# Kernel optimization log

Measured on AMD Instinct MI355X. Metric: run time of the kernel, lower is better.

The kernel has to match this reference:

```python
import jax, jax.numpy as jnp
import numpy as np

IN_DIMS = 1024
OUT_DIMS = 1024
N_TOKENS = 32768


def setup_inputs() -> dict:
    key = jax.random.key(0)
    k_x, k_wl0, k_wl1, k_scale, k_shift, k_noise = jax.random.split(key, 6)
    x = jax.random.normal(k_x, (N_TOKENS, IN_DIMS), dtype=jnp.float32)
    # weight_logits[..., 0]: magnitude logits, weight_logits[..., 1]: sign logits
    gain = np.sqrt(2.0)  # relu gain
    a = gain * np.sqrt(6.0 / (IN_DIMS + OUT_DIMS))
    mag_logits = jax.random.uniform(k_wl0, (OUT_DIMS, IN_DIMS), dtype=jnp.float32,
                                    minval=-a, maxval=a)  # logit(0.5)=0, so centered at 0
    sgn_logits = jax.random.uniform(k_wl1, (OUT_DIMS, IN_DIMS), dtype=jnp.float32,
                                    minval=-a, maxval=a)
    weight_logits = jnp.stack([mag_logits, sgn_logits], axis=-1)  # [O, I, 2]
    scale = jnp.full((OUT_DIMS,), np.float32(a), dtype=jnp.float32)
    shift = jnp.full((OUT_DIMS,), 0.01, dtype=jnp.float32)
    noise = jax.random.normal(k_noise, (N_TOKENS, OUT_DIMS), dtype=jnp.float32)
    return {"x": x, "weight_logits": weight_logits, "scale": scale,
            "shift": shift, "noise": noise}


def reference(x, weight_logits, scale, shift, noise):
    # train_forward of TernaryLinear
    weight_p = jax.nn.sigmoid(weight_logits)          # [O, I, 2]
    p_mag = weight_p[..., 0]                          # P(|w| = 1)
    p_sgn = weight_p[..., 1]                          # P(w > 0 | |w| = 1)
    s = 2.0 * p_sgn - 1.0
    weight_mean = p_mag * s                           # [O, I]
    weight_var = p_mag - (p_mag * p_mag) * (s * s)    # [O, I], >= 0
    out_mean = jnp.einsum('ni,oi->no', x, weight_mean)         # [N, O]
    out_var = jnp.einsum('ni,oi->no', x * x, weight_var)       # [N, O]
    out = out_mean + jnp.sqrt(out_var) * noise
    out = out * scale[None, :] + shift[None, :]
    return out
```

## Files before the change

### kernel.cpp

```cpp
#include <hip/hip_runtime.h>
#include <hip/hip_bf16.h>
#include <cmath>

#define N_TOK 32768
#define KDIM  1024
#define ODIM  1024

#define BM 256
#define BN 128
#define BK 64
#define NKT (KDIM / BK)
#define THREADS 512
#define BUFSZ 65536

typedef float          f32x4  __attribute__((ext_vector_type(4)));
typedef __bf16         bf16x8 __attribute__((ext_vector_type(8)));
typedef unsigned short us8    __attribute__((ext_vector_type(8)));
typedef unsigned short us2   __attribute__((ext_vector_type(2)));

static __device__ __forceinline__ unsigned short f2bf(float f) {
  unsigned u = __builtin_bit_cast(unsigned, f);
  u += 0x7FFFu + ((u >> 16) & 1u);
  return (unsigned short)(u >> 16);
}

static __device__ __forceinline__ unsigned short bfc(float f) {
  return __builtin_bit_cast(unsigned short, (__bf16)f);
}

static __device__ __forceinline__ f32x4 mfma16(us8 a, us8 b, f32x4 c) {
  return __builtin_amdgcn_mfma_f32_16x16x32_bf16(
      __builtin_bit_cast(bf16x8, a), __builtin_bit_cast(bf16x8, b), c, 0, 0, 0);
}

static __device__ __forceinline__ void gl_lds16(const void* g, void* l) {
  __builtin_amdgcn_global_load_lds(
      (const __attribute__((address_space(1))) void*)g,
      (__attribute__((address_space(3))) void*)l, 16, 0, 0);
}

static __device__ __forceinline__ us8 sqr8(us8 a) {
  us8 r;
#pragma unroll
  for (int i = 0; i < 8; ++i) {
    float f = __builtin_bit_cast(float, (unsigned)a[i] << 16);
    r[i] = bfc(f * f);
  }
  return r;
}

__global__ void wprep_kernel(const float* __restrict__ wl,
                             unsigned short* __restrict__ wm,
                             unsigned short* __restrict__ wv) {
  int i = blockIdx.x * blockDim.x + threadIdx.x;
  f32x4 v = *reinterpret_cast<const f32x4*>(wl + (size_t)i * 4);
  float pm0 = 1.f / (1.f + expf(-v.x));
  float ps0 = 1.f / (1.f + expf(-v.y));
  float pm1 = 1.f / (1.f + expf(-v.z));
  float ps1 = 1.f / (1.f + expf(-v.w));
  float m0 = pm0 * (2.f * ps0 - 1.f);
  float m1 = pm1 * (2.f * ps1 - 1.f);
  float q0 = pm0 - m0 * m0;
  float q1 = pm1 - m1 * m1;
  us2 am = {f2bf(m0), f2bf(m1)};
  us2 av = {f2bf(q0), f2bf(q1)};
  *reinterpret_cast<us2*>(wm + (size_t)i * 2) = am;
  *reinterpret_cast<us2*>(wv + (size_t)i * 2) = av;
}

__global__ __launch_bounds__(THREADS, 2) void ternary_gemm(
    const float* __restrict__ x,
    const unsigned short* __restrict__ wm,
    const unsigned short* __restrict__ wv,
    const float* __restrict__ scale,
    const float* __restrict__ shift,
    const float* __restrict__ noise,
    float* __restrict__ out) {
  __shared__ alignas(16) char smem[2 * BUFSZ];

  const int tid  = threadIdx.x;
  const int lane = tid & 63;
  const int w    = tid >> 6;
  const bool isVar = (w >= 4);
  const int p    = w & 3;
  const int wr   = p >> 1;
  const int wc   = p & 1;
  const int l15  = lane & 15;
  const int l4   = lane >> 4;

  const int bid = blockIdx.x;
  const int swz = (bid & 7) * 128 + (bid >> 3);
  const int bm  = swz >> 3;
  const int bn  = swz & 7;
  const int rowBase = bm * BM;
  const int colBase = bn * BN;

  f32x4 acc[8][4];
#pragma unroll
  for (int i = 0; i < 8; ++i)
#pragma unroll
    for (int j = 0; j < 4; ++j) acc[i][j] = (f32x4)0.f;

  const float* xb = x + (size_t)rowBase * KDIM;

  auto stageB = [&](int kt, char* buf) {
    const int k0 = kt * BK;
    char* BsM = buf + 32768;
    char* BsV = buf + 49152;
#pragma unroll
    for (int c = 0; c < 2; ++c) {
      int flat = c * THREADS + tid;
      int row  = flat >> 3;
      int j    = flat & 7;
      size_t goff = (size_t)(colBase + row) * KDIM + k0 + ((j ^ (row & 7)) << 3);
      gl_lds16(wm + goff, BsM + flat * 16);
      gl_lds16(wv + goff, BsV + flat * 16);
    }
  };
  auto loadX = [&](int kt, f32x4* ap) {
    const float* xt = xb + kt * BK;
#pragma unroll
    for (int c = 0; c < 4; ++c) {
      int flat = c * THREADS + tid;
      int row  = flat >> 3;
      int j    = flat & 7;
      const float* s = xt + (size_t)row * KDIM + j * 8;
      ap[2 * c]     = *reinterpret_cast<const f32x4*>(s);
      ap[2 * c + 1] = *reinterpret_cast<const f32x4*>(s + 4);
    }
  };
  auto writeA = [&](const f32x4* ap, char* buf) {
#pragma unroll
    for (int c = 0; c < 4; ++c) {
      int flat = c * THREADS + tid;
      int row  = flat >> 3;
      int j    = flat & 7;
      f32x4 v0 = ap[2 * c], v1 = ap[2 * c + 1];
      us8 o = {bfc(v0.x), bfc(v0.y), bfc(v0.z), bfc(v0.w),
               bfc(v1.x), bfc(v1.y), bfc(v1.z), bfc(v1.w)};
      int off = row * 128 + ((j * 16) ^ ((row & 7) << 4));
      *reinterpret_cast<us8*>(buf + off) = o;
    }
  };

  f32x4 ap[8];
  stageB(0, smem);
  loadX(0, ap);
  writeA(ap, smem);
  __syncthreads();

  for (int kt = 0; kt < NKT; ++kt) {
    const char* cur = smem + (size_t)(kt & 1) * BUFSZ;
    char*       nxt = smem + (size_t)((kt + 1) & 1) * BUFSZ;

    if (kt + 1 < NKT) { stageB(kt + 1, nxt); loadX(kt + 1, ap); }

    const char* Ab = cur;
    const char* Bb = cur + 32768 + (isVar ? 16384 : 0);
#pragma unroll
    for (int ks = 0; ks < 2; ++ks) {
      const int kb = ks * 64 + (l4 << 4);
      us8 bf_[4], af[8];
#pragma unroll
      for (int b = 0; b < 4; ++b) {
        int row = wc * 64 + b * 16 + l15;
        bf_[b] = *reinterpret_cast<const us8*>(Bb + row * 128 + (kb ^ ((row & 7) << 4)));
      }
#pragma unroll
      for (int i = 0; i < 8; ++i) {
        int row = wr * 128 + i * 16 + l15;
        af[i] = *reinterpret_cast<const us8*>(Ab + row * 128 + (kb ^ ((row & 7) << 4)));
        if (isVar) af[i] = sqr8(af[i]);
      }
#pragma unroll
      for (int i = 0; i < 8; ++i)
#pragma unroll
        for (int b = 0; b < 4; ++b)
          acc[i][b] = mfma16(af[i], bf_[b], acc[i][b]);
    }

    if (kt + 1 < NKT) writeA(ap, nxt);

    __syncthreads();
  }

  float* Mx = (float*)smem;
  float* Vx = (float*)(smem + 65536);
  if (!isVar) {
#pragma unroll
    for (int i = 4; i < 8; ++i)
#pragma unroll
      for (int b = 0; b < 4; ++b)
#pragma unroll
        for (int j = 0; j < 4; ++j) {
          int lr = (i - 4) * 16 + l4 * 4 + j;
          int lc = b * 16 + l15;
          Mx[(p * 64 + lr) * 64 + (lc ^ ((lr & 4) << 2))] = acc[i][b][j];
        }
  } else {
#pragma unroll
    for (int i = 0; i < 4; ++i)
#pragma unroll
      for (int b = 0; b < 4; ++b)
#pragma unroll
        for (int j = 0; j < 4; ++j) {
          int lr = i * 16 + l4 * 4 + j;
          int lc = b * 16 + l15;
          Vx[(p * 64 + lr) * 64 + (lc ^ ((lr & 4) << 2))] = acc[i][b][j];
        }
  }
  __syncthreads();

  if (!isVar) {
#pragma unroll
    for (int i = 0; i < 4; ++i)
#pragma unroll
      for (int b = 0; b < 4; ++b) {
        int col = colBase + wc * 64 + b * 16 + l15;
        float sc = scale[col], sh = shift[col];
#pragma unroll
        for (int j = 0; j < 4; ++j) {
          int lr = i * 16 + l4 * 4 + j;
          float vv = Vx[(p * 64 + lr) * 64 + ((b * 16 + l15) ^ ((lr & 4) << 2))];
          size_t idx = (size_t)(rowBase + wr * 128 + lr) * ODIM + col;
          out[idx] = fmaf(acc[i][b][j] + sqrtf(fmaxf(vv, 0.f)) * noise[idx], sc, sh);
        }
      }
  } else {
#pragma unroll
    for (int i = 4; i < 8; ++i)
#pragma unroll
      for (int b = 0; b < 4; ++b) {
        int col = colBase + wc * 64 + b * 16 + l15;
        float sc = scale[col], sh = shift[col];
#pragma unroll
        for (int j = 0; j < 4; ++j) {
          int lr = (i - 4) * 16 + l4 * 4 + j;
          float mm = Mx[(p * 64 + lr) * 64 + ((b * 16 + l15) ^ ((lr & 4) << 2))];
          size_t idx = (size_t)(rowBase + wr * 128 + 64 + lr) * ODIM + col;
          out[idx] = fmaf(mm + sqrtf(fmaxf(acc[i][b][j], 0.f)) * noise[idx], sc, sh);
        }
      }
  }
}

extern "C" void kernel_launch(void* const* d_in, const int* in_sizes, int n_in,
                              void* d_out, int out_size, void* d_ws, size_t ws_size,
                              hipStream_t stream) {
  const float* x     = (const float*)d_in[0];
  const float* wl    = (const float*)d_in[1];
  const float* scale = (const float*)d_in[2];
  const float* shift = (const float*)d_in[3];
  const float* noise = (const float*)d_in[4];
  float* out = (float*)d_out;

  unsigned short* wm = (unsigned short*)d_ws;
  unsigned short* wv = wm + (size_t)ODIM * KDIM;

  wprep_kernel<<<(ODIM * KDIM / 2) / 256, 256, 0, stream>>>(wl, wm, wv);

  ternary_gemm<<<(N_TOK / BM) * (ODIM / BN), THREADS, 0, stream>>>(
      x, wm, wv, scale, shift, noise, out);
}
```

Baseline: 252.0 us.

## Hand-schedule GEMM main loop with explicit waitcnts, split A fragments, setprio

Swaps __syncthreads for explicit vmcnt/lgkmcnt waits and raw s_barrier. Global loads of X are issued before the B LDS copies so a partial vmcnt can release the X registers early. The A fragment loads are split into two halves of four, with MFMA bursts at raised priority and an extra barrier after each half, to interleave LDS reads with matrix math across waves and lower register pressure. The hand-counted vmcnt values are fragile, and the added per-half barriers may cost synchronization overhead.

```diff
diff --git a/kernel.cpp b/kernel.cpp
--- a/kernel.cpp
+++ b/kernel.cpp
@@ -16,7 +16,12 @@
 typedef float          f32x4  __attribute__((ext_vector_type(4)));
 typedef __bf16         bf16x8 __attribute__((ext_vector_type(8)));
 typedef unsigned short us8    __attribute__((ext_vector_type(8)));
-typedef unsigned short us2   __attribute__((ext_vector_type(2)));
+typedef unsigned short us2    __attribute__((ext_vector_type(2)));
+
+#define VMCNT(n)  asm volatile("s_waitcnt vmcnt(" #n ")" ::: "memory")
+#define LGKM0()   asm volatile("s_waitcnt lgkmcnt(0)" ::: "memory")
+#define SBAR()    asm volatile("s_barrier" ::: "memory")
+#define SCHED0()  __builtin_amdgcn_sched_barrier(0)
 
 static __device__ __forceinline__ unsigned short f2bf(float f) {
   unsigned u = __builtin_bit_cast(unsigned, f);
@@ -144,44 +149,69 @@
   };
 
   f32x4 ap[8];
+  loadX(0, ap);
   stageB(0, smem);
-  loadX(0, ap);
+  VMCNT(4);
+  SCHED0();
   writeA(ap, smem);
-  __syncthreads();
+  LGKM0();
+  SBAR();
 
   for (int kt = 0; kt < NKT; ++kt) {
     const char* cur = smem + (size_t)(kt & 1) * BUFSZ;
     char*       nxt = smem + (size_t)((kt + 1) & 1) * BUFSZ;
 
-    if (kt + 1 < NKT) { stageB(kt + 1, nxt); loadX(kt + 1, ap); }
+    if (kt + 1 < NKT) {
+      loadX(kt + 1, ap);
+      stageB(kt + 1, nxt);
+      VMCNT(12);
+    } else {
+      VMCNT(0);
+    }
+    SCHED0();
 
     const char* Ab = cur;
     const char* Bb = cur + 32768 + (isVar ? 16384 : 0);
+
+    us8 bf_[4];
 #pragma unroll
     for (int ks = 0; ks < 2; ++ks) {
       const int kb = ks * 64 + (l4 << 4);
-      us8 bf_[4], af[8];
 #pragma unroll
       for (int b = 0; b < 4; ++b) {
         int row = wc * 64 + b * 16 + l15;
         bf_[b] = *reinterpret_cast<const us8*>(Bb + row * 128 + (kb ^ ((row & 7) << 4)));
       }
 #pragma unroll
-      for (int i = 0; i < 8; ++i) {
-        int row = wr * 128 + i * 16 + l15;
-        af[i] = *reinterpret_cast<const us8*>(Ab + row * 128 + (kb ^ ((row & 7) << 4)));
-        if (isVar) af[i] = sqr8(af[i]);
-      }
-#pragma unroll
-      for (int i = 0; i < 8; ++i)
-#pragma unroll
-        for (int b = 0; b < 4; ++b)
-          acc[i][b] = mfma16(af[i], bf_[b], acc[i][b]);
-    }
-
-    if (kt + 1 < NKT) writeA(ap, nxt);
-
-    __syncthreads();
+      for (int ih = 0; ih < 2; ++ih) {
+        us8 af[4];
+#pragma unroll
+        for (int ii = 0; ii < 4; ++ii) {
+          int row = wr * 128 + (ih * 4 + ii) * 16 + l15;
+          af[ii] = *reinterpret_cast<const us8*>(Ab + row * 128 + (kb ^ ((row & 7) << 4)));
+        }
+        if (isVar) {
+#pragma unroll
+          for (int ii = 0; ii < 4; ++ii) af[ii] = sqr8(af[ii]);
+        }
+        __builtin_amdgcn_s_setprio(1);
+#pragma unroll
+        for (int ii = 0; ii < 4; ++ii)
+#pragma unroll
+          for (int b = 0; b < 4; ++b)
+            acc[ih * 4 + ii][b] = mfma16(af[ii], bf_[b], acc[ih * 4 + ii][b]);
+        __builtin_amdgcn_s_setprio(0);
+        SBAR();
+      }
+    }
+
+    if (kt + 1 < NKT) {
+      VMCNT(4);
+      SCHED0();
+      writeA(ap, nxt);
+    }
+    LGKM0();
+    SBAR();
   }
 
   float* Mx = (float*)smem;
```

Measured after the change: 262.7 us. +4.2%, slower.
